# Kernel tuning notes

Measured on AMD Instinct MI355X. Metric: run time of the kernel, lower is better.

The kernel has to match this reference:

```python
import jax, jax.numpy as jnp
import numpy as np
import math

HIDDEN = 1024
HEADS = 16
HEAD_DIM = HIDDEN // HEADS
TEMP_K = 1000.0  # custom temperature multiplier applied after masking
B, S = 2, 2048


def setup_inputs() -> dict:
    key = jax.random.key(0)
    ks = jax.random.split(key, 4)
    scale = 1.0 / math.sqrt(HIDDEN)
    return {
        "x": jax.random.normal(ks[0], (B, S, HIDDEN), dtype=jnp.float32),
        "W_qkv": jax.random.normal(ks[1], (HIDDEN, 3 * HIDDEN), dtype=jnp.float32) * scale,
        "b_qkv": jnp.zeros((3 * HIDDEN,), dtype=jnp.float32),
        "W_out": jax.random.normal(ks[2], (HIDDEN, HIDDEN), dtype=jnp.float32) * scale,
        "b_out": jnp.zeros((HIDDEN,), dtype=jnp.float32),
    }


def reference(x, W_qkv, b_qkv, W_out, b_out):
    b, s, _ = x.shape
    qkv = x @ W_qkv + b_qkv                                    # [b,s,3*hidden]
    qkv = qkv.reshape(b, s, 3, HEADS, HEAD_DIM)
    qkv = jnp.transpose(qkv, (2, 0, 3, 1, 4))                  # [3,b,h,s,d]
    q, k, v = qkv[0], qkv[1], qkv[2]
    scores = jnp.einsum('bhqd,bhkd->bhqk', q, k) / math.sqrt(HEAD_DIM)
    causal = jnp.tril(jnp.ones((s, s), dtype=bool))            # [s,s]
    scores = jnp.where(causal[None, None], scores, -jnp.inf)
    probs = jax.nn.softmax(scores * TEMP_K, axis=-1)           # temp-scaled softmax
    attn = jnp.einsum('bhqk,bhkd->bhqd', probs, v)             # [b,h,s,d]
    attn = jnp.transpose(attn, (0, 2, 1, 3)).reshape(b, s, HIDDEN)
    return attn @ W_out + b_out
```

## Files before the change

kernel.cpp:

```cpp
#include <hip/hip_runtime.h>
#include <hip/hip_bf16.h>

#define BATCH 2
#define SEQ 2048
#define HID 1024
#define NHEAD 16
#define HDIM 64
#define LSCALE 125.0f
#define NEGBIG (-1.0e30f)
#define N_ITEMS 512

typedef __bf16 bf16;
typedef __bf16 bf16x4 __attribute__((ext_vector_type(4)));
typedef __bf16 bf16x8 __attribute__((ext_vector_type(8)));
typedef float f32x16 __attribute__((ext_vector_type(16)));

__global__ __launch_bounds__(256) void transpose_split_kernel(
    const float* __restrict__ W, bf16* __restrict__ Thi, bf16* __restrict__ Tlo,
    int K, int N)
{
    __shared__ float T[64][65];
    const int tid = threadIdx.x;
    const int kBase = blockIdx.y * 64;
    const int nBase = blockIdx.x * 64;
    {
        const int k0 = tid >> 4;
        const int nc = (tid & 15) * 4;
#pragma unroll
        for (int kk = 0; kk < 4; kk++) {
            int k = k0 + kk * 16;
            float4 v = *(const float4*)(W + (size_t)(kBase + k) * N + nBase + nc);
            T[k][nc] = v.x; T[k][nc + 1] = v.y; T[k][nc + 2] = v.z; T[k][nc + 3] = v.w;
        }
    }
    __syncthreads();
    {
        const int n = tid >> 2;
        const int kc = (tid & 3) * 16;
        bf16x8 h0, h1, l0, l1;
#pragma unroll
        for (int j = 0; j < 8; j++) {
            float a = T[kc + j][n];
            float c = T[kc + 8 + j][n];
            bf16 ha = (bf16)a, hc = (bf16)c;
            h0[j] = ha; h1[j] = hc;
            l0[j] = (bf16)(a - (float)ha);
            l1[j] = (bf16)(c - (float)hc);
        }
        size_t dst = (size_t)(nBase + n) * K + kBase + kc;
        *(bf16x8*)(Thi + dst)     = h0;
        *(bf16x8*)(Thi + dst + 8) = h1;
        if (Tlo) {
            *(bf16x8*)(Tlo + dst)     = l0;
            *(bf16x8*)(Tlo + dst + 8) = l1;
        }
    }
}

__global__ __launch_bounds__(256) void xsplit_kernel(
    const float* __restrict__ X, bf16* __restrict__ Xhi, bf16* __restrict__ Xlo,
    unsigned* __restrict__ ctr)
{
    if (blockIdx.x == 0 && threadIdx.x == 0) *ctr = 0u;
    const int i = blockIdx.x * 256 + threadIdx.x;
    float4 v = ((const float4*)X)[i];
    float xs[4] = {v.x, v.y, v.z, v.w};
    bf16x4 h, l;
#pragma unroll
    for (int j = 0; j < 4; j++) {
        h[j] = (bf16)xs[j];
        l[j] = (bf16)(xs[j] - (float)h[j]);
    }
    ((bf16x4*)Xhi)[i] = h;
    ((bf16x4*)Xlo)[i] = l;
}

__global__ __launch_bounds__(256) void gemm_qkv_mfma(
    const bf16* __restrict__ Xhi, const bf16* __restrict__ Xlo,
    const bf16* __restrict__ Wthi, const bf16* __restrict__ Wtlo,
    const float* __restrict__ bias,
    bf16* __restrict__ qhi, bf16* __restrict__ qlo,
    bf16* __restrict__ khi, bf16* __restrict__ klo, bf16* __restrict__ vv)
{
    __shared__ __align__(16) bf16 Xh[128][40];
    __shared__ __align__(16) bf16 Xl[128][40];
    __shared__ __align__(16) bf16 Wh[128][40];
    __shared__ __align__(16) bf16 Wl[128][40];

    const int tid = threadIdx.x;
    const int wave = tid >> 6, lane = tid & 63;
    const int lm = lane & 31, lq2 = lane >> 5;
    const int wave_s = wave & 1, wave_n = wave >> 1;
    const int nBase = blockIdx.x * 128;
    const int sBase = blockIdx.y * 128;
    const bool isV = (nBase >= 2 * HID);

    const int sr = tid >> 1, skc = (tid & 1) * 16;

    f32x16 acc[2][2];
#pragma unroll
    for (int st = 0; st < 2; st++)
#pragma unroll
      for (int nt = 0; nt < 2; nt++)
#pragma unroll
        for (int r = 0; r < 16; r++) acc[st][nt][r] = 0.f;

    for (int k0 = 0; k0 < HID; k0 += 32) {
        size_t xsrc = (size_t)(sBase + sr) * HID + k0 + skc;
        size_t wsrc = (size_t)(nBase + sr) * HID + k0 + skc;
        bf16x8 xh0 = *(const bf16x8*)(Xhi + xsrc);
        bf16x8 xh1 = *(const bf16x8*)(Xhi + xsrc + 8);
        bf16x8 wh0 = *(const bf16x8*)(Wthi + wsrc);
        bf16x8 wh1 = *(const bf16x8*)(Wthi + wsrc + 8);
        bf16x8 xl0 = {}, xl1 = {}, wl0 = {}, wl1 = {};
        if (!isV) {
            xl0 = *(const bf16x8*)(Xlo + xsrc);
            xl1 = *(const bf16x8*)(Xlo + xsrc + 8);
            wl0 = *(const bf16x8*)(Wtlo + wsrc);
            wl1 = *(const bf16x8*)(Wtlo + wsrc + 8);
        }
        __syncthreads();
        *(bf16x8*)&Xh[sr][skc]     = xh0;
        *(bf16x8*)&Xh[sr][skc + 8] = xh1;
        *(bf16x8*)&Wh[sr][skc]     = wh0;
        *(bf16x8*)&Wh[sr][skc + 8] = wh1;
        if (!isV) {
            *(bf16x8*)&Xl[sr][skc]     = xl0;
            *(bf16x8*)&Xl[sr][skc + 8] = xl1;
            *(bf16x8*)&Wl[sr][skc]     = wl0;
            *(bf16x8*)&Wl[sr][skc + 8] = wl1;
        }
        __syncthreads();

#pragma unroll
        for (int kh = 0; kh < 2; kh++) {
            const int ko = kh * 16 + lq2 * 8;
            bf16x8 aWh[2], aWl[2], bXh[2], bXl[2];
#pragma unroll
            for (int nt = 0; nt < 2; nt++) {
                aWh[nt] = *(bf16x8*)&Wh[wave_n * 64 + nt * 32 + lm][ko];
                if (!isV) aWl[nt] = *(bf16x8*)&Wl[wave_n * 64 + nt * 32 + lm][ko];
            }
#pragma unroll
            for (int st = 0; st < 2; st++) {
                bXh[st] = *(bf16x8*)&Xh[wave_s * 64 + st * 32 + lm][ko];
                if (!isV) bXl[st] = *(bf16x8*)&Xl[wave_s * 64 + st * 32 + lm][ko];
            }
#pragma unroll
            for (int nt = 0; nt < 2; nt++)
#pragma unroll
              for (int st = 0; st < 2; st++) {
                acc[st][nt] = __builtin_amdgcn_mfma_f32_32x32x16_bf16(aWh[nt], bXh[st], acc[st][nt], 0, 0, 0);
                if (!isV) {
                    acc[st][nt] = __builtin_amdgcn_mfma_f32_32x32x16_bf16(aWh[nt], bXl[st], acc[st][nt], 0, 0, 0);
                    acc[st][nt] = __builtin_amdgcn_mfma_f32_32x32x16_bf16(aWl[nt], bXh[st], acc[st][nt], 0, 0, 0);
                }
              }
        }
    }

#pragma unroll
    for (int st = 0; st < 2; st++) {
        int s = sBase + wave_s * 64 + st * 32 + lm;
        int bb = s >> 11, ss = s & 2047;
#pragma unroll
        for (int nt = 0; nt < 2; nt++) {
#pragma unroll
            for (int q4 = 0; q4 < 4; q4++) {
                int n = nBase + wave_n * 64 + nt * 32 + 8 * q4 + 4 * lq2;
                float4 bv = *(const float4*)(bias + n);
                float vals[4];
                vals[0] = acc[st][nt][q4 * 4 + 0] + bv.x;
                vals[1] = acc[st][nt][q4 * 4 + 1] + bv.y;
                vals[2] = acc[st][nt][q4 * 4 + 2] + bv.z;
                vals[3] = acc[st][nt][q4 * 4 + 3] + bv.w;
                int which = n >> 10, h = (n >> 6) & 15, d = n & 63;
                size_t dst = (((size_t)bb * NHEAD + h) * SEQ + ss) * HDIM + d;
                if (which < 2) {
                    bf16x4 hi4, lo4;
#pragma unroll
                    for (int i = 0; i < 4; i++) {
                        hi4[i] = (bf16)vals[i];
                        lo4[i] = (bf16)(vals[i] - (float)hi4[i]);
                    }
                    bf16* ph = (which == 0) ? qhi : khi;
                    bf16* pl = (which == 0) ? qlo : klo;
                    *(bf16x4*)(ph + dst) = hi4;
                    *(bf16x4*)(pl + dst) = lo4;
                } else {
                    bf16x4 v4;
#pragma unroll
                    for (int i = 0; i < 4; i++) v4[i] = (bf16)vals[i];
                    *(bf16x4*)(vv + dst) = v4;
                }
            }
        }
    }
}

__global__ __launch_bounds__(256) void attn_kernel(
    const bf16* __restrict__ Qhi, const bf16* __restrict__ Qlo,
    const bf16* __restrict__ Khg, const bf16* __restrict__ Klg,
    const bf16* __restrict__ Vg, bf16* __restrict__ attnbuf,
    unsigned* __restrict__ ctr)
{
    __shared__ __align__(16) bf16 Khs[64][72];
    __shared__ __align__(16) bf16 Kls[64][72];
    __shared__ __align__(16) bf16 Vt [64][72];
    __shared__ __align__(16) bf16 Pb [128][72];
    __shared__ int s_item;

    const int tid  = threadIdx.x;
    const int wave = tid >> 6;
    const int lane = tid & 63;
    const int lm   = lane & 31;
    const int lq2  = lane >> 5;

    const int kr  = tid >> 2;
    const int kd0 = (tid & 3) * 16;
    const int vd  = tid & 63;
    const int vc0 = (tid >> 6) * 16;

    for (;;) {
        if (tid == 0) s_item = (int)atomicAdd(ctr, 1u);
        __syncthreads();
        const int it = s_item;
        if (it >= N_ITEMS) return;
        const int qt = 15 - (it >> 5);
        const int bh = it & 31;
        const int b = bh >> 4, h = bh & 15;
        const size_t headoff = ((size_t)b * NHEAD + h) * SEQ * HDIM;

        const int qg = qt * 128 + wave * 32 + lm;
        bf16x8 qh[4], ql[4];
        {
            const bf16* qph = Qhi + headoff + (size_t)qg * HDIM;
            const bf16* qpl = Qlo + headoff + (size_t)qg * HDIM;
#pragma unroll
            for (int c = 0; c < 4; c++) {
                qh[c] = *(const bf16x8*)(qph + c * 16 + lq2 * 8);
                ql[c] = *(const bf16x8*)(qpl + c * 16 + lq2 * 8);
            }
        }

        f32x16 O0, O1;
#pragma unroll
        for (int r = 0; r < 16; r++) { O0[r] = 0.f; O1[r] = 0.f; }
        float m_run = NEGBIG, l_run = 0.f;

        const int ktmax = 2 * qt + 1;
        for (int kt = 0; kt <= ktmax; kt++) {
            size_t kbase_g = headoff + (size_t)(kt * 64 + kr) * HDIM + kd0;
            bf16x8 kh0 = *(const bf16x8*)(Khg + kbase_g);
            bf16x8 kh1 = *(const bf16x8*)(Khg + kbase_g + 8);
            bf16x8 kl0 = *(const bf16x8*)(Klg + kbase_g);
            bf16x8 kl1 = *(const bf16x8*)(Klg + kbase_g + 8);
            bf16 vtmp[16];
#pragma unroll
            for (int i = 0; i < 16; i++)
                vtmp[i] = Vg[headoff + (size_t)(kt * 64 + vc0 + i) * HDIM + vd];

            __syncthreads();

            *(bf16x8*)&Khs[kr][kd0]     = kh0;
            *(bf16x8*)&Khs[kr][kd0 + 8] = kh1;
            *(bf16x8*)&Kls[kr][kd0]     = kl0;
            *(bf16x8*)&Kls[kr][kd0 + 8] = kl1;
            {
                bf16x8 v0, v1;
#pragma unroll
                for (int i = 0; i < 8; i++) { v0[i] = vtmp[i]; v1[i] = vtmp[i + 8]; }
                *(bf16x8*)&Vt[vd][vc0]     = v0;
                *(bf16x8*)&Vt[vd][vc0 + 8] = v1;
            }
            __syncthreads();

            f32x16 s0, s1;
#pragma unroll
            for (int r = 0; r < 16; r++) { s0[r] = 0.f; s1[r] = 0.f; }
#pragma unroll
            for (int c = 0; c < 4; c++) {
                bf16x8 ah0 = *(bf16x8*)&Khs[lm][c * 16 + lq2 * 8];
                bf16x8 al0 = *(bf16x8*)&Kls[lm][c * 16 + lq2 * 8];
                bf16x8 ah1 = *(bf16x8*)&Khs[32 + lm][c * 16 + lq2 * 8];
                bf16x8 al1 = *(bf16x8*)&Kls[32 + lm][c * 16 + lq2 * 8];
                s0 = __builtin_amdgcn_mfma_f32_32x32x16_bf16(ah0, qh[c], s0, 0, 0, 0);
                s0 = __builtin_amdgcn_mfma_f32_32x32x16_bf16(ah0, ql[c], s0, 0, 0, 0);
                s0 = __builtin_amdgcn_mfma_f32_32x32x16_bf16(al0, qh[c], s0, 0, 0, 0);
                s1 = __builtin_amdgcn_mfma_f32_32x32x16_bf16(ah1, qh[c], s1, 0, 0, 0);
                s1 = __builtin_amdgcn_mfma_f32_32x32x16_bf16(ah1, ql[c], s1, 0, 0, 0);
                s1 = __builtin_amdgcn_mfma_f32_32x32x16_bf16(al1, qh[c], s1, 0, 0, 0);
            }

            float logit[2][16];
            const int kbase = kt * 64 + 4 * lq2;
            const bool needmask = (kt * 64 + 63 > qg);
#pragma unroll
            for (int r = 0; r < 16; r++) {
                int koff = (r & 3) + 8 * (r >> 2);
                float L0 = s0[r] * LSCALE;
                float L1 = s1[r] * LSCALE;
                if (needmask) {
                    if (kbase + koff > qg) L0 = NEGBIG;
                    if (kbase + 32 + koff > qg) L1 = NEGBIG;
                }
                logit[0][r] = L0;
                logit[1][r] = L1;
            }

            float vmax = NEGBIG;
#pragma unroll
            for (int r = 0; r < 16; r++)
                vmax = fmaxf(vmax, fmaxf(logit[0][r], logit[1][r]));
            vmax = fmaxf(vmax, __shfl_xor(vmax, 32, 64));
            float mnew = fmaxf(m_run, vmax);
            float alpha = __expf(m_run - mnew);
            float p[2][16];
            float sum = 0.f;
#pragma unroll
            for (int r = 0; r < 16; r++) {
                p[0][r] = __expf(logit[0][r] - mnew);
                p[1][r] = __expf(logit[1][r] - mnew);
                sum += p[0][r] + p[1][r];
            }
            sum += __shfl_xor(sum, 32, 64);
            l_run = l_run * alpha + sum;
            m_run = mnew;
#pragma unroll
            for (int r = 0; r < 16; r++) { O0[r] *= alpha; O1[r] *= alpha; }

#pragma unroll
            for (int mt = 0; mt < 2; mt++)
#pragma unroll
              for (int g = 0; g < 4; g++) {
                bf16x4 pk;
                pk[0] = (bf16)p[mt][4 * g + 0];
                pk[1] = (bf16)p[mt][4 * g + 1];
                pk[2] = (bf16)p[mt][4 * g + 2];
                pk[3] = (bf16)p[mt][4 * g + 3];
                *(bf16x4*)&Pb[wave * 32 + lm][mt * 32 + 8 * g + 4 * lq2] = pk;
              }
            asm volatile("s_waitcnt lgkmcnt(0)" ::: "memory");

#pragma unroll
            for (int c = 0; c < 4; c++) {
                bf16x8 pb  = *(bf16x8*)&Pb[wave * 32 + lm][c * 16 + lq2 * 8];
                bf16x8 va0 = *(bf16x8*)&Vt[lm][c * 16 + lq2 * 8];
                bf16x8 va1 = *(bf16x8*)&Vt[32 + lm][c * 16 + lq2 * 8];
                O0 = __builtin_amdgcn_mfma_f32_32x32x16_bf16(va0, pb, O0, 0, 0, 0);
                O1 = __builtin_amdgcn_mfma_f32_32x32x16_bf16(va1, pb, O1, 0, 0, 0);
            }
        }

        const float inv = 1.0f / l_run;
        bf16* orow = attnbuf + ((size_t)b * SEQ + qg) * HID + h * HDIM;
#pragma unroll
        for (int g = 0; g < 4; g++) {
            int d0 = 8 * g + 4 * lq2;
            bf16x4 o0, o1;
#pragma unroll
            for (int i = 0; i < 4; i++) {
                o0[i] = (bf16)(O0[4 * g + i] * inv);
                o1[i] = (bf16)(O1[4 * g + i] * inv);
            }
            *(bf16x4*)(orow + d0)      = o0;
            *(bf16x4*)(orow + 32 + d0) = o1;
        }
    }
}

__global__ __launch_bounds__(256) void gemm_out_mfma(
    const bf16* __restrict__ Attn, const bf16* __restrict__ Wt,
    const float* __restrict__ bias, float* __restrict__ out)
{
    __shared__ __align__(16) bf16 Ah[64][40];
    __shared__ __align__(16) bf16 Bh[128][40];

    const int tid = threadIdx.x;
    const int wave = tid >> 6, lane = tid & 63;
    const int lm = lane & 31, lq2 = lane >> 5;
    const int nBase = blockIdx.x * 64;
    const int mBase = blockIdx.y * 128;

    const int sr = tid >> 1, skc = (tid & 1) * 16;
    const int ar = tid >> 2, akc = (tid & 3) * 8;

    f32x16 acc[2];
#pragma unroll
    for (int nt = 0; nt < 2; nt++)
#pragma unroll
      for (int r = 0; r < 16; r++) acc[nt][r] = 0.f;

    for (int k0 = 0; k0 < HID; k0 += 32) {
        size_t bsrc = (size_t)(mBase + sr) * HID + k0 + skc;
        size_t asrc = (size_t)(nBase + ar) * HID + k0 + akc;
        bf16x8 b0 = *(const bf16x8*)(Attn + bsrc);
        bf16x8 b1 = *(const bf16x8*)(Attn + bsrc + 8);
        bf16x8 a0 = *(const bf16x8*)(Wt + asrc);
        __syncthreads();
        *(bf16x8*)&Bh[sr][skc]     = b0;
        *(bf16x8*)&Bh[sr][skc + 8] = b1;
        *(bf16x8*)&Ah[ar][akc]     = a0;
        __syncthreads();
#pragma unroll
        for (int kh = 0; kh < 2; kh++) {
            const int ko = kh * 16 + lq2 * 8;
            bf16x8 bA  = *(bf16x8*)&Bh[wave * 32 + lm][ko];
            bf16x8 aW0 = *(bf16x8*)&Ah[lm][ko];
            bf16x8 aW1 = *(bf16x8*)&Ah[32 + lm][ko];
            acc[0] = __builtin_amdgcn_mfma_f32_32x32x16_bf16(aW0, bA, acc[0], 0, 0, 0);
            acc[1] = __builtin_amdgcn_mfma_f32_32x32x16_bf16(aW1, bA, acc[1], 0, 0, 0);
        }
    }

    const int m = mBase + wave * 32 + lm;
#pragma unroll
    for (int nt = 0; nt < 2; nt++) {
#pragma unroll
        for (int q4 = 0; q4 < 4; q4++) {
            int n = nBase + nt * 32 + 8 * q4 + 4 * lq2;
            float4 bv = *(const float4*)(bias + n);
            float4 o;
            o.x = acc[nt][q4 * 4 + 0] + bv.x;
            o.y = acc[nt][q4 * 4 + 1] + bv.y;
            o.z = acc[nt][q4 * 4 + 2] + bv.z;
            o.w = acc[nt][q4 * 4 + 3] + bv.w;
            *(float4*)(out + (size_t)m * HID + n) = o;
        }
    }
}

extern "C" void kernel_launch(void* const* d_in, const int* in_sizes, int n_in,
                              void* d_out, int out_size, void* d_ws, size_t ws_size,
                              hipStream_t stream) {
    const float* x    = (const float*)d_in[0];
    const float* Wqkv = (const float*)d_in[1];
    const float* bqkv = (const float*)d_in[2];
    const float* Wout = (const float*)d_in[3];
    const float* bout = (const float*)d_in[4];
    float* out = (float*)d_out;

    const size_t NW  = (size_t)HID * 3 * HID;
    const size_t NWo = (size_t)HID * HID;
    const size_t NT  = (size_t)BATCH * NHEAD * SEQ * HDIM;
    bf16* Wthi = (bf16*)d_ws;
    bf16* Wtlo = Wthi + NW;
    bf16* Wot  = Wtlo + NW;
    bf16* qhi  = Wot + NWo;
    bf16* qlo  = qhi + NT;
    bf16* khi  = qlo + NT;
    bf16* klo  = khi + NT;
    bf16* vv   = klo + NT;
    bf16* attnbuf = vv + NT;
    bf16* Xhi  = attnbuf;
    bf16* Xlo  = attnbuf + NT;
    unsigned* ctr = (unsigned*)(Xlo + NT);

    xsplit_kernel<<<dim3((BATCH * SEQ * HID) / 1024), 256, 0, stream>>>(x, Xhi, Xlo, ctr);
    transpose_split_kernel<<<dim3(3 * HID / 64, HID / 64), 256, 0, stream>>>(
        Wqkv, Wthi, Wtlo, HID, 3 * HID);
    transpose_split_kernel<<<dim3(HID / 64, HID / 64), 256, 0, stream>>>(
        Wout, Wot, nullptr, HID, HID);
    gemm_qkv_mfma<<<dim3(3 * HID / 128, BATCH * SEQ / 128), 256, 0, stream>>>(
        Xhi, Xlo, Wthi, Wtlo, bqkv, qhi, qlo, khi, klo, vv);
    attn_kernel<<<dim3(768), 256, 0, stream>>>(
        qhi, qlo, khi, klo, vv, attnbuf, ctr);
    gemm_out_mfma<<<dim3(HID / 64, BATCH * SEQ / 128), 256, 0, stream>>>(
        attnbuf, Wot, bout, out);
}
```

Before: 298.7 us.

## Prefetch next tiles in GEMMs and attention, pre-transpose V, shuffle P in registers

Both GEMM kernels now double-buffer in registers: the next K-slab is loaded from global memory while the MFMAs for the current slab run. A new kernel pre-transposes V so attention loads V tiles with vector loads instead of strided scalar gathers. Attention also prefetches the next K/V tile and skips fully masked tiles per wave. It builds the P operand with cross-lane shuffles instead of a shared-memory round trip and uses exp2 with a folded scale. Costs are an extra kernel launch and higher register pressure, and the attention grid grows to 1024 blocks.

```diff
diff --git a/kernel.cpp b/kernel.cpp
--- a/kernel.cpp
+++ b/kernel.cpp
@@ -6,7 +6,7 @@
 #define HID 1024
 #define NHEAD 16
 #define HDIM 64
-#define LSCALE 125.0f
+#define L2SCALE 180.3368800721f
 #define NEGBIG (-1.0e30f)
 #define N_ITEMS 512
 
@@ -14,6 +14,9 @@
 typedef __bf16 bf16x4 __attribute__((ext_vector_type(4)));
 typedef __bf16 bf16x8 __attribute__((ext_vector_type(8)));
 typedef float f32x16 __attribute__((ext_vector_type(16)));
+
+union BQ  { bf16x4 v; unsigned u[2]; };
+union BF8 { bf16x8 v; unsigned u[4]; };
 
 __global__ __launch_bounds__(256) void transpose_split_kernel(
     const float* __restrict__ W, bf16* __restrict__ Thi, bf16* __restrict__ Tlo,
@@ -75,6 +78,32 @@
     ((bf16x4*)Xlo)[i] = l;
 }
 
+__global__ __launch_bounds__(256) void vtrans_kernel(
+    const bf16* __restrict__ vv, bf16* __restrict__ vtr)
+{
+    __shared__ bf16 T[64][72];
+    const int tid = threadIdx.x;
+    const int bh = blockIdx.y;
+    const int st = blockIdx.x;
+    const int r  = tid >> 2;
+    const int c0 = (tid & 3) * 16;
+    const bf16* src = vv + ((size_t)bh * SEQ + st * 64) * HDIM;
+    bf16x8 a = *(const bf16x8*)(src + (size_t)r * HDIM + c0);
+    bf16x8 b = *(const bf16x8*)(src + (size_t)r * HDIM + c0 + 8);
+    *(bf16x8*)&T[r][c0]     = a;
+    *(bf16x8*)&T[r][c0 + 8] = b;
+    __syncthreads();
+    bf16x8 o0, o1;
+#pragma unroll
+    for (int i = 0; i < 8; i++) {
+        o0[i] = T[c0 + i][r];
+        o1[i] = T[c0 + 8 + i][r];
+    }
+    bf16* dst = vtr + ((size_t)bh * HDIM + r) * SEQ + st * 64 + c0;
+    *(bf16x8*)(dst)     = o0;
+    *(bf16x8*)(dst + 8) = o1;
+}
+
 __global__ __launch_bounds__(256) void gemm_qkv_mfma(
     const bf16* __restrict__ Xhi, const bf16* __restrict__ Xlo,
     const bf16* __restrict__ Wthi, const bf16* __restrict__ Wtlo,
@@ -105,32 +134,51 @@
 #pragma unroll
         for (int r = 0; r < 16; r++) acc[st][nt][r] = 0.f;
 
+    bf16x8 cx[2], cw[2], cxl[2] = {}, cwl[2] = {};
+    {
+        size_t xsrc = (size_t)(sBase + sr) * HID + skc;
+        size_t wsrc = (size_t)(nBase + sr) * HID + skc;
+        cx[0] = *(const bf16x8*)(Xhi + xsrc);
+        cx[1] = *(const bf16x8*)(Xhi + xsrc + 8);
+        cw[0] = *(const bf16x8*)(Wthi + wsrc);
+        cw[1] = *(const bf16x8*)(Wthi + wsrc + 8);
+        if (!isV) {
+            cxl[0] = *(const bf16x8*)(Xlo + xsrc);
+            cxl[1] = *(const bf16x8*)(Xlo + xsrc + 8);
+            cwl[0] = *(const bf16x8*)(Wtlo + wsrc);
+            cwl[1] = *(const bf16x8*)(Wtlo + wsrc + 8);
+        }
+    }
+
     for (int k0 = 0; k0 < HID; k0 += 32) {
-        size_t xsrc = (size_t)(sBase + sr) * HID + k0 + skc;
-        size_t wsrc = (size_t)(nBase + sr) * HID + k0 + skc;
-        bf16x8 xh0 = *(const bf16x8*)(Xhi + xsrc);
-        bf16x8 xh1 = *(const bf16x8*)(Xhi + xsrc + 8);
-        bf16x8 wh0 = *(const bf16x8*)(Wthi + wsrc);
-        bf16x8 wh1 = *(const bf16x8*)(Wthi + wsrc + 8);
-        bf16x8 xl0 = {}, xl1 = {}, wl0 = {}, wl1 = {};
+        __syncthreads();
+        *(bf16x8*)&Xh[sr][skc]     = cx[0];
+        *(bf16x8*)&Xh[sr][skc + 8] = cx[1];
+        *(bf16x8*)&Wh[sr][skc]     = cw[0];
+        *(bf16x8*)&Wh[sr][skc + 8] = cw[1];
         if (!isV) {
-            xl0 = *(const bf16x8*)(Xlo + xsrc);
-            xl1 = *(const bf16x8*)(Xlo + xsrc + 8);
-            wl0 = *(const bf16x8*)(Wtlo + wsrc);
-            wl1 = *(const bf16x8*)(Wtlo + wsrc + 8);
+            *(bf16x8*)&Xl[sr][skc]     = cxl[0];
+            *(bf16x8*)&Xl[sr][skc + 8] = cxl[1];
+            *(bf16x8*)&Wl[sr][skc]     = cwl[0];
+            *(bf16x8*)&Wl[sr][skc + 8] = cwl[1];
         }
         __syncthreads();
-        *(bf16x8*)&Xh[sr][skc]     = xh0;
-        *(bf16x8*)&Xh[sr][skc + 8] = xh1;
-        *(bf16x8*)&Wh[sr][skc]     = wh0;
-        *(bf16x8*)&Wh[sr][skc + 8] = wh1;
-        if (!isV) {
-            *(bf16x8*)&Xl[sr][skc]     = xl0;
-            *(bf16x8*)&Xl[sr][skc + 8] = xl1;
-            *(bf16x8*)&Wl[sr][skc]     = wl0;
-            *(bf16x8*)&Wl[sr][skc + 8] = wl1;
-        }
-        __syncthreads();
+
+        bf16x8 nx[2] = {}, nw[2] = {}, nxl[2] = {}, nwl[2] = {};
+        if (k0 + 32 < HID) {
+            size_t xsrc = (size_t)(sBase + sr) * HID + k0 + 32 + skc;
+            size_t wsrc = (size_t)(nBase + sr) * HID + k0 + 32 + skc;
+            nx[0] = *(const bf16x8*)(Xhi + xsrc);
+            nx[1] = *(const bf16x8*)(Xhi + xsrc + 8);
+            nw[0] = *(const bf16x8*)(Wthi + wsrc);
+            nw[1] = *(const bf16x8*)(Wthi + wsrc + 8);
+            if (!isV) {
+                nxl[0] = *(const bf16x8*)(Xlo + xsrc);
+                nxl[1] = *(const bf16x8*)(Xlo + xsrc + 8);
+                nwl[0] = *(const bf16x8*)(Wtlo + wsrc);
+                nwl[1] = *(const bf16x8*)(Wtlo + wsrc + 8);
+            }
+        }
 
 #pragma unroll
         for (int kh = 0; kh < 2; kh++) {
@@ -157,6 +205,8 @@
                 }
               }
         }
+        cx[0] = nx[0]; cx[1] = nx[1]; cw[0] = nw[0]; cw[1] = nw[1];
+        cxl[0] = nxl[0]; cxl[1] = nxl[1]; cwl[0] = nwl[0]; cwl[1] = nwl[1];
     }
 
 #pragma unroll
@@ -201,13 +251,12 @@
 __global__ __launch_bounds__(256) void attn_kernel(
     const bf16* __restrict__ Qhi, const bf16* __restrict__ Qlo,
     const bf16* __restrict__ Khg, const bf16* __restrict__ Klg,
-    const bf16* __restrict__ Vg, bf16* __restrict__ attnbuf,
+    const bf16* __restrict__ Vtr, bf16* __restrict__ attnbuf,
     unsigned* __restrict__ ctr)
 {
     __shared__ __align__(16) bf16 Khs[64][72];
     __shared__ __align__(16) bf16 Kls[64][72];
     __shared__ __align__(16) bf16 Vt [64][72];
-    __shared__ __align__(16) bf16 Pb [128][72];
     __shared__ int s_item;
 
     const int tid  = threadIdx.x;
@@ -218,8 +267,6 @@
 
     const int kr  = tid >> 2;
     const int kd0 = (tid & 3) * 16;
-    const int vd  = tid & 63;
-    const int vc0 = (tid >> 6) * 16;
 
     for (;;) {
         if (tid == 0) s_item = (int)atomicAdd(ctr, 1u);
@@ -249,106 +296,128 @@
         float m_run = NEGBIG, l_run = 0.f;
 
         const int ktmax = 2 * qt + 1;
+        bf16x8 kc[4], vc[2];
+        {
+            size_t kg = headoff + (size_t)kr * HDIM + kd0;
+            kc[0] = *(const bf16x8*)(Khg + kg);
+            kc[1] = *(const bf16x8*)(Khg + kg + 8);
+            kc[2] = *(const bf16x8*)(Klg + kg);
+            kc[3] = *(const bf16x8*)(Klg + kg + 8);
+            size_t vg = headoff + (size_t)kr * SEQ + kd0;
+            vc[0] = *(const bf16x8*)(Vtr + vg);
+            vc[1] = *(const bf16x8*)(Vtr + vg + 8);
+        }
+
         for (int kt = 0; kt <= ktmax; kt++) {
-            size_t kbase_g = headoff + (size_t)(kt * 64 + kr) * HDIM + kd0;
-            bf16x8 kh0 = *(const bf16x8*)(Khg + kbase_g);
-            bf16x8 kh1 = *(const bf16x8*)(Khg + kbase_g + 8);
-            bf16x8 kl0 = *(const bf16x8*)(Klg + kbase_g);
-            bf16x8 kl1 = *(const bf16x8*)(Klg + kbase_g + 8);
-            bf16 vtmp[16];
-#pragma unroll
-            for (int i = 0; i < 16; i++)
-                vtmp[i] = Vg[headoff + (size_t)(kt * 64 + vc0 + i) * HDIM + vd];
-
             __syncthreads();
-
-            *(bf16x8*)&Khs[kr][kd0]     = kh0;
-            *(bf16x8*)&Khs[kr][kd0 + 8] = kh1;
-            *(bf16x8*)&Kls[kr][kd0]     = kl0;
-            *(bf16x8*)&Kls[kr][kd0 + 8] = kl1;
-            {
-                bf16x8 v0, v1;
-#pragma unroll
-                for (int i = 0; i < 8; i++) { v0[i] = vtmp[i]; v1[i] = vtmp[i + 8]; }
-                *(bf16x8*)&Vt[vd][vc0]     = v0;
-                *(bf16x8*)&Vt[vd][vc0 + 8] = v1;
-            }
+            *(bf16x8*)&Khs[kr][kd0]     = kc[0];
+            *(bf16x8*)&Khs[kr][kd0 + 8] = kc[1];
+            *(bf16x8*)&Kls[kr][kd0]     = kc[2];
+            *(bf16x8*)&Kls[kr][kd0 + 8] = kc[3];
+            *(bf16x8*)&Vt[kr][kd0]      = vc[0];
+            *(bf16x8*)&Vt[kr][kd0 + 8]  = vc[1];
             __syncthreads();
 
-            f32x16 s0, s1;
-#pragma unroll
-            for (int r = 0; r < 16; r++) { s0[r] = 0.f; s1[r] = 0.f; }
-#pragma unroll
-            for (int c = 0; c < 4; c++) {
-                bf16x8 ah0 = *(bf16x8*)&Khs[lm][c * 16 + lq2 * 8];
-                bf16x8 al0 = *(bf16x8*)&Kls[lm][c * 16 + lq2 * 8];
-                bf16x8 ah1 = *(bf16x8*)&Khs[32 + lm][c * 16 + lq2 * 8];
-                bf16x8 al1 = *(bf16x8*)&Kls[32 + lm][c * 16 + lq2 * 8];
-                s0 = __builtin_amdgcn_mfma_f32_32x32x16_bf16(ah0, qh[c], s0, 0, 0, 0);
-                s0 = __builtin_amdgcn_mfma_f32_32x32x16_bf16(ah0, ql[c], s0, 0, 0, 0);
-                s0 = __builtin_amdgcn_mfma_f32_32x32x16_bf16(al0, qh[c], s0, 0, 0, 0);
-                s1 = __builtin_amdgcn_mfma_f32_32x32x16_bf16(ah1, qh[c], s1, 0, 0, 0);
-                s1 = __builtin_amdgcn_mfma_f32_32x32x16_bf16(ah1, ql[c], s1, 0, 0, 0);
-                s1 = __builtin_amdgcn_mfma_f32_32x32x16_bf16(al1, qh[c], s1, 0, 0, 0);
-            }
-
-            float logit[2][16];
-            const int kbase = kt * 64 + 4 * lq2;
-            const bool needmask = (kt * 64 + 63 > qg);
-#pragma unroll
-            for (int r = 0; r < 16; r++) {
-                int koff = (r & 3) + 8 * (r >> 2);
-                float L0 = s0[r] * LSCALE;
-                float L1 = s1[r] * LSCALE;
-                if (needmask) {
-                    if (kbase + koff > qg) L0 = NEGBIG;
-                    if (kbase + 32 + koff > qg) L1 = NEGBIG;
+            bf16x8 kn[4], vn[2];
+            const bool more = (kt < ktmax);
+            if (more) {
+                size_t kg = headoff + (size_t)((kt + 1) * 64 + kr) * HDIM + kd0;
+                kn[0] = *(const bf16x8*)(Khg + kg);
+                kn[1] = *(const bf16x8*)(Khg + kg + 8);
+                kn[2] = *(const bf16x8*)(Klg + kg);
+                kn[3] = *(const bf16x8*)(Klg + kg + 8);
+                size_t vg = headoff + (size_t)kr * SEQ + (kt + 1) * 64 + kd0;
+                vn[0] = *(const bf16x8*)(Vtr + vg);
+                vn[1] = *(const bf16x8*)(Vtr + vg + 8);
+            }
+
+            if (kt * 64 <= qt * 128 + wave * 32 + 31) {
+                f32x16 s[2];
+#pragma unroll
+                for (int r = 0; r < 16; r++) { s[0][r] = 0.f; s[1][r] = 0.f; }
+#pragma unroll
+                for (int c = 0; c < 4; c++) {
+                    bf16x8 ah0 = *(bf16x8*)&Khs[lm][c * 16 + lq2 * 8];
+                    bf16x8 al0 = *(bf16x8*)&Kls[lm][c * 16 + lq2 * 8];
+                    bf16x8 ah1 = *(bf16x8*)&Khs[32 + lm][c * 16 + lq2 * 8];
+                    bf16x8 al1 = *(bf16x8*)&Kls[32 + lm][c * 16 + lq2 * 8];
+                    s[0] = __builtin_amdgcn_mfma_f32_32x32x16_bf16(ah0, qh[c], s[0], 0, 0, 0);
+                    s[0] = __builtin_amdgcn_mfma_f32_32x32x16_bf16(ah0, ql[c], s[0], 0, 0, 0);
+                    s[0] = __builtin_amdgcn_mfma_f32_32x32x16_bf16(al0, qh[c], s[0], 0, 0, 0);
+                    s[1] = __builtin_amdgcn_mfma_f32_32x32x16_bf16(ah1, qh[c], s[1], 0, 0, 0);
+                    s[1] = __builtin_amdgcn_mfma_f32_32x32x16_bf16(ah1, ql[c], s[1], 0, 0, 0);
+                    s[1] = __builtin_amdgcn_mfma_f32_32x32x16_bf16(al1, qh[c], s[1], 0, 0, 0);
                 }
-                logit[0][r] = L0;
-                logit[1][r] = L1;
-            }
-
-            float vmax = NEGBIG;
-#pragma unroll
-            for (int r = 0; r < 16; r++)
-                vmax = fmaxf(vmax, fmaxf(logit[0][r], logit[1][r]));
-            vmax = fmaxf(vmax, __shfl_xor(vmax, 32, 64));
-            float mnew = fmaxf(m_run, vmax);
-            float alpha = __expf(m_run - mnew);
-            float p[2][16];
-            float sum = 0.f;
-#pragma unroll
-            for (int r = 0; r < 16; r++) {
-                p[0][r] = __expf(logit[0][r] - mnew);
-                p[1][r] = __expf(logit[1][r] - mnew);
-                sum += p[0][r] + p[1][r];
-            }
-            sum += __shfl_xor(sum, 32, 64);
-            l_run = l_run * alpha + sum;
-            m_run = mnew;
-#pragma unroll
-            for (int r = 0; r < 16; r++) { O0[r] *= alpha; O1[r] *= alpha; }
-
-#pragma unroll
-            for (int mt = 0; mt < 2; mt++)
-#pragma unroll
-              for (int g = 0; g < 4; g++) {
-                bf16x4 pk;
-                pk[0] = (bf16)p[mt][4 * g + 0];
-                pk[1] = (bf16)p[mt][4 * g + 1];
-                pk[2] = (bf16)p[mt][4 * g + 2];
-                pk[3] = (bf16)p[mt][4 * g + 3];
-                *(bf16x4*)&Pb[wave * 32 + lm][mt * 32 + 8 * g + 4 * lq2] = pk;
-              }
-            asm volatile("s_waitcnt lgkmcnt(0)" ::: "memory");
-
-#pragma unroll
-            for (int c = 0; c < 4; c++) {
-                bf16x8 pb  = *(bf16x8*)&Pb[wave * 32 + lm][c * 16 + lq2 * 8];
-                bf16x8 va0 = *(bf16x8*)&Vt[lm][c * 16 + lq2 * 8];
-                bf16x8 va1 = *(bf16x8*)&Vt[32 + lm][c * 16 + lq2 * 8];
-                O0 = __builtin_amdgcn_mfma_f32_32x32x16_bf16(va0, pb, O0, 0, 0, 0);
-                O1 = __builtin_amdgcn_mfma_f32_32x32x16_bf16(va1, pb, O1, 0, 0, 0);
+
+                const int kbase = kt * 64 + 4 * lq2;
+                const bool needmask = (kt * 64 + 63 > qg);
+#pragma unroll
+                for (int mt = 0; mt < 2; mt++)
+#pragma unroll
+                  for (int r = 0; r < 16; r++) {
+                    int koff = (r & 3) + 8 * (r >> 2) + 32 * mt;
+                    float L = s[mt][r] * L2SCALE;
+                    if (needmask && (kbase + koff > qg)) L = NEGBIG;
+                    s[mt][r] = L;
+                  }
+
+                float vmax = NEGBIG;
+#pragma unroll
+                for (int r = 0; r < 16; r++)
+                    vmax = fmaxf(vmax, fmaxf(s[0][r], s[1][r]));
+                vmax = fmaxf(vmax, __shfl_xor(vmax, 32, 64));
+                float mnew = fmaxf(m_run, vmax);
+                float alpha = exp2f(m_run - mnew);
+                float sum = 0.f;
+#pragma unroll
+                for (int mt = 0; mt < 2; mt++)
+#pragma unroll
+                  for (int r = 0; r < 16; r++) {
+                    s[mt][r] = exp2f(s[mt][r] - mnew);
+                    sum += s[mt][r];
+                  }
+                sum += __shfl_xor(sum, 32, 64);
+                l_run = l_run * alpha + sum;
+                m_run = mnew;
+#pragma unroll
+                for (int r = 0; r < 16; r++) { O0[r] *= alpha; O1[r] *= alpha; }
+
+                bf16x8 pfrag[4];
+#pragma unroll
+                for (int mt = 0; mt < 2; mt++)
+#pragma unroll
+                  for (int hh = 0; hh < 2; hh++) {
+                    BQ A, B;
+#pragma unroll
+                    for (int i = 0; i < 4; i++) {
+                        A.v[i] = (bf16)s[mt][8 * hh + i];
+                        B.v[i] = (bf16)s[mt][8 * hh + 4 + i];
+                    }
+                    unsigned s0_ = lq2 ? A.u[0] : B.u[0];
+                    unsigned s1_ = lq2 ? A.u[1] : B.u[1];
+                    unsigned r0 = __shfl_xor(s0_, 32, 64);
+                    unsigned r1 = __shfl_xor(s1_, 32, 64);
+                    BF8 f;
+                    f.u[0] = lq2 ? r0 : A.u[0];
+                    f.u[1] = lq2 ? r1 : A.u[1];
+                    f.u[2] = lq2 ? B.u[0] : r0;
+                    f.u[3] = lq2 ? B.u[1] : r1;
+                    pfrag[mt * 2 + hh] = f.v;
+                  }
+
+#pragma unroll
+                for (int c = 0; c < 4; c++) {
+                    bf16x8 va0 = *(bf16x8*)&Vt[lm][c * 16 + lq2 * 8];
+                    bf16x8 va1 = *(bf16x8*)&Vt[32 + lm][c * 16 + lq2 * 8];
+                    O0 = __builtin_amdgcn_mfma_f32_32x32x16_bf16(va0, pfrag[c], O0, 0, 0, 0);
+                    O1 = __builtin_amdgcn_mfma_f32_32x32x16_bf16(va1, pfrag[c], O1, 0, 0, 0);
+                }
+            }
+
+            if (more) {
+#pragma unroll
+                for (int i = 0; i < 4; i++) kc[i] = kn[i];
+                vc[0] = vn[0]; vc[1] = vn[1];
             }
         }
 
@@ -391,17 +460,26 @@
 #pragma unroll
       for (int r = 0; r < 16; r++) acc[nt][r] = 0.f;
 
+    bf16x8 cb[2], ca;
+    {
+        cb[0] = *(const bf16x8*)(Attn + (size_t)(mBase + sr) * HID + skc);
+        cb[1] = *(const bf16x8*)(Attn + (size_t)(mBase + sr) * HID + skc + 8);
+        ca    = *(const bf16x8*)(Wt + (size_t)(nBase + ar) * HID + akc);
+    }
+
     for (int k0 = 0; k0 < HID; k0 += 32) {
-        size_t bsrc = (size_t)(mBase + sr) * HID + k0 + skc;
-        size_t asrc = (size_t)(nBase + ar) * HID + k0 + akc;
-        bf16x8 b0 = *(const bf16x8*)(Attn + bsrc);
-        bf16x8 b1 = *(const bf16x8*)(Attn + bsrc + 8);
-        bf16x8 a0 = *(const bf16x8*)(Wt + asrc);
         __syncthreads();
-        *(bf16x8*)&Bh[sr][skc]     = b0;
-        *(bf16x8*)&Bh[sr][skc + 8] = b1;
-        *(bf16x8*)&Ah[ar][akc]     = a0;
+        *(bf16x8*)&Bh[sr][skc]     = cb[0];
+        *(bf16x8*)&Bh[sr][skc + 8] = cb[1];
+        *(bf16x8*)&Ah[ar][akc]     = ca;
         __syncthreads();
+
+        bf16x8 nb[2] = {}, na = {};
+        if (k0 + 32 < HID) {
+            nb[0] = *(const bf16x8*)(Attn + (size_t)(mBase + sr) * HID + k0 + 32 + skc);
+            nb[1] = *(const bf16x8*)(Attn + (size_t)(mBase + sr) * HID + k0 + 32 + skc + 8);
+            na    = *(const bf16x8*)(Wt + (size_t)(nBase + ar) * HID + k0 + 32 + akc);
+        }
 #pragma unroll
         for (int kh = 0; kh < 2; kh++) {
             const int ko = kh * 16 + lq2 * 8;
@@ -411,6 +489,7 @@
             acc[0] = __builtin_amdgcn_mfma_f32_32x32x16_bf16(aW0, bA, acc[0], 0, 0, 0);
             acc[1] = __builtin_amdgcn_mfma_f32_32x32x16_bf16(aW1, bA, acc[1], 0, 0, 0);
         }
+        cb[0] = nb[0]; cb[1] = nb[1]; ca = na;
     }
 
     const int m = mBase + wave * 32 + lm;
@@ -454,6 +533,7 @@
     bf16* attnbuf = vv + NT;
     bf16* Xhi  = attnbuf;
     bf16* Xlo  = attnbuf + NT;
+    bf16* vtr  = Xlo;
     unsigned* ctr = (unsigned*)(Xlo + NT);
 
     xsplit_kernel<<<dim3((BATCH * SEQ * HID) / 1024), 256, 0, stream>>>(x, Xhi, Xlo, ctr);
@@ -463,8 +543,9 @@
         Wout, Wot, nullptr, HID, HID);
     gemm_qkv_mfma<<<dim3(3 * HID / 128, BATCH * SEQ / 128), 256, 0, stream>>>(
         Xhi, Xlo, Wthi, Wtlo, bqkv, qhi, qlo, khi, klo, vv);
-    attn_kernel<<<dim3(768), 256, 0, stream>>>(
-        qhi, qlo, khi, klo, vv, attnbuf, ctr);
+    vtrans_kernel<<<dim3(SEQ / 64, BATCH * NHEAD), 256, 0, stream>>>(vv, vtr);
+    attn_kernel<<<dim3(1024), 256, 0, stream>>>(
+        qhi, qlo, khi, klo, vtr, attnbuf, ctr);
     gemm_out_mfma<<<dim3(HID / 64, BATCH * SEQ / 128), 256, 0, stream>>>(
         attnbuf, Wot, bout, out);
 }
```

Result: faster. 277.4 us (-7.1%).
